# Performance work log

Hardware: AMD Instinct MI355X
Metric: run time of the kernel (lower is better)

Reference implementation:

```python
import jax, jax.numpy as jnp
import numpy as np

B, L, S, H, E = 4, 2048, 2048, 8, 64

def setup_inputs() -> dict:
    key = jax.random.key(0)
    kq, kk, kv, kt, kd = jax.random.split(key, 5)
    return {
        "queries": jax.random.normal(kq, (B, L, H, E), dtype=jnp.float32),
        "keys": jax.random.normal(kk, (B, S, H, E), dtype=jnp.float32),
        "values": jax.random.normal(kv, (B, S, H, E), dtype=jnp.float32),
        "attn_mask": jnp.zeros((1,), dtype=bool),
        "tau": jax.random.uniform(kt, (B, 1), dtype=jnp.float32),
        "delta": jax.random.normal(kd, (B, 1), dtype=jnp.float32),
    }

def reference(queries, keys, values, attn_mask, tau, delta):
    # queries: [B,L,H,E], keys: [B,S,H,E], values: [B,S,H,D]
    Bq, Lq, Hq, Eq = queries.shape
    scale = 1.0 / jnp.sqrt(jnp.float32(Eq))
    scores = jnp.einsum('blhe,bshe->bhls', queries, keys)  # [B,H,L,S]
    scores = scores * tau.reshape(Bq, 1, 1, 1)             # per-batch tau scale
    scores = scores + delta.reshape(Bq, 1, 1, 1)           # per-batch delta bias
    A = jax.nn.softmax(scale * scores, axis=-1)            # dropout is identity at eval
    V = jnp.einsum('bhls,bshd->blhd', A, values)           # [B,L,H,D]
    return V
```

## Files before the change

### kernel.cpp

```cpp
#include <hip/hip_runtime.h>
#include <hip/hip_bf16.h>
#include <stdint.h>

#define LL 2048
#define SS 2048
#define HH 8
#define EE 64
#define RSG 512

typedef float v4f __attribute__((ext_vector_type(4)));
typedef short s4v __attribute__((ext_vector_type(4)));
typedef short s8v __attribute__((ext_vector_type(8)));

__device__ __forceinline__ short f2bf(float f) {
    unsigned u = __float_as_uint(f);
    u = (u + 0x7fffu + ((u >> 16) & 1u)) >> 16;
    return (short)u;
}

__device__ __forceinline__ s4v pack4bf(float a, float b, float c, float d) {
    float2 ab = make_float2(a, b), cd = make_float2(c, d);
    __hip_bfloat162 r0 = __float22bfloat162_rn(ab);
    __hip_bfloat162 r1 = __float22bfloat162_rn(cd);
    s4v r;
    __builtin_memcpy(&r, &r0, 4);
    __builtin_memcpy(((char*)&r) + 4, &r1, 4);
    return r;
}

__global__ __launch_bounds__(256)
void dsattn_prep(const float* __restrict__ kk, const float* __restrict__ vv,
                 short* __restrict__ kbf, short* __restrict__ vimg)
{
    __shared__ float T[64][68];
    const int t = threadIdx.x;
    const int blk = blockIdx.x;
    if (blk < 1024) {
        const float* src = kk + (size_t)blk * 4096;
        short* dst = kbf + (size_t)blk * 4096;
        #pragma unroll
        for (int c = 0; c < 4; ++c) {
            v4f d = *(const v4f*)(src + (c * 256 + t) * 4);
            *(s4v*)(dst + (c * 256 + t) * 4) = pack4bf(d[0], d[1], d[2], d[3]);
        }
    } else {
        const int vb = blk - 1024;
        const int b = vb >> 8, h = (vb >> 5) & 7, ts = vb & 31;
        const float* vp = vv + ((size_t)b * SS + ts * 64) * RSG + h * EE;
        #pragma unroll
        for (int c = 0; c < 4; ++c) {
            int idx = c * 256 + t, s = idx >> 4, e0 = (idx & 15) << 2;
            *(v4f*)&T[s][e0] = *(const v4f*)(vp + (size_t)s * RSG + e0);
        }
        __syncthreads();
        short* dst = vimg + (size_t)vb * 4096;
        #pragma unroll
        for (int half = 0; half < 2; ++half) {
            int ci = half * 256 + t;
            int e = ci >> 3, sc = ci & 7;
            int c = sc ^ (e & 7);
            s8v ov;
            #pragma unroll
            for (int m = 0; m < 8; ++m) {
                int s = 16 * (m & 3) + 2 * c + (m >> 2);
                ov[m] = f2bf(T[s][e]);
            }
            *(s8v*)(dst + ci * 8) = ov;
        }
    }
}

__global__ __launch_bounds__(256, 2)
void dsattn_main(const float* __restrict__ q, const short* __restrict__ kbf,
                 const short* __restrict__ vimg, const float* __restrict__ tau,
                 const float* __restrict__ delta, float* __restrict__ out)
{
    __shared__ short KV[2][8192];
    __shared__ short Ps[128 * 64];

    const int t    = threadIdx.x;
    const int lane = t & 63;
    const int w    = t >> 6;
    const int l15  = lane & 15;
    const int l4   = lane >> 4;
    const int mt = blockIdx.x, h = blockIdx.y, b = blockIdx.z;

    const float LOG2E = 1.44269504088896f;
    const float sc2 = 0.125f * LOG2E * tau[b];
    const float dl2 = 0.125f * LOG2E * delta[b];

    s8v qf[2][2];
    {
        const float* qb = q + ((size_t)b * LL + (size_t)mt * 128 + w * 32) * RSG + h * EE;
        #pragma unroll
        for (int mb = 0; mb < 2; ++mb) {
            const float* qr = qb + (size_t)(mb * 16 + l15) * RSG + l4 * 8;
            v4f a0 = *(const v4f*)(qr);
            v4f a1 = *(const v4f*)(qr + 4);
            v4f a2 = *(const v4f*)(qr + 32);
            v4f a3 = *(const v4f*)(qr + 36);
            s4v p0 = pack4bf(a0[0], a0[1], a0[2], a0[3]);
            s4v p1 = pack4bf(a1[0], a1[1], a1[2], a1[3]);
            s4v p2 = pack4bf(a2[0], a2[1], a2[2], a2[3]);
            s4v p3 = pack4bf(a3[0], a3[1], a3[2], a3[3]);
            s8v f0, f1;
            #pragma unroll
            for (int j = 0; j < 4; ++j) { f0[j] = p0[j]; f0[4 + j] = p1[j]; f1[j] = p2[j]; f1[4 + j] = p3[j]; }
            qf[mb][0] = f0; qf[mb][1] = f1;
        }
    }

    const char* gsrc;
    int jstr, tstr;
    if (w < 2) {
        int i = w * 256 + lane;
        int row = i >> 3;
        int c = (i & 7) ^ (row & 7);
        gsrc = (const char*)(kbf + (size_t)b * (SS * RSG) + h * EE) + row * (RSG * 2) + c * 16;
        jstr = 8 * RSG * 2;
        tstr = 64 * RSG * 2;
    } else {
        int i2 = (w - 2) * 256 + lane;
        gsrc = (const char*)(vimg + (((size_t)b * HH + h) * 32) * 4096) + i2 * 16;
        jstr = 1024; tstr = 8192;
    }

    #define STAGE(p)                                                                    \
        {                                                                               \
            _Pragma("unroll")                                                           \
            for (int j = 0; j < 4; ++j) {                                               \
                __builtin_amdgcn_global_load_lds(                                       \
                    (const __attribute__((address_space(1))) unsigned*)(gsrc + j * jstr), \
                    (__attribute__((address_space(3))) unsigned*)&KV[p][w * 2048 + j * 512], \
                    16, 0, 0);                                                          \
            }                                                                           \
            gsrc += tstr;                                                               \
        }

    v4f oacc[2][4];
    float rs[2][4];
    #pragma unroll
    for (int mb = 0; mb < 2; ++mb)
        #pragma unroll
        for (int nb = 0; nb < 4; ++nb) {
            v4f z = {0.f, 0.f, 0.f, 0.f};
            oacc[mb][nb] = z;
            rs[mb][nb] = 0.f;
        }

    STAGE(0);

    for (int it = 0; it < 32; ++it) {
        const int p = it & 1;
        __syncthreads();
        if (it < 31) STAGE(p ^ 1);

        const short* Kp = &KV[p][0];
        const short* Vp = &KV[p][4096];

        v4f st[2][4];
        #pragma unroll
        for (int sb = 0; sb < 4; ++sb) {
            int sr = l15 + 16 * sb;
            int xo = sr & 7;
            s8v b0 = *(const s8v*)&Kp[sr * 64 + ((l4 ^ xo) << 3)];
            s8v b1 = *(const s8v*)&Kp[sr * 64 + (((l4 + 4) ^ xo) << 3)];
            #pragma unroll
            for (int mb = 0; mb < 2; ++mb) {
                v4f z = {0.f, 0.f, 0.f, 0.f};
                v4f a = __builtin_amdgcn_mfma_f32_16x16x32_bf16(qf[mb][0], b0, z, 0, 0, 0);
                st[mb][sb] = __builtin_amdgcn_mfma_f32_16x16x32_bf16(qf[mb][1], b1, a, 0, 0, 0);
            }
        }

        #pragma unroll
        for (int mb = 0; mb < 2; ++mb) {
            #pragma unroll
            for (int sb = 0; sb < 4; ++sb)
                #pragma unroll
                for (int r = 0; r < 4; ++r)
                    st[mb][sb][r] = __builtin_amdgcn_exp2f(st[mb][sb][r] * sc2 + dl2);
            #pragma unroll
            for (int r = 0; r < 4; ++r) {
                rs[mb][r] += (st[mb][0][r] + st[mb][1][r]) + (st[mb][2][r] + st[mb][3][r]);
                s4v pk = pack4bf(st[mb][0][r], st[mb][1][r], st[mb][2][r], st[mb][3][r]);
                int prow = w * 32 + mb * 16 + (l4 << 2) + r;
                int sc = (l15 >> 1) ^ (prow & 7);
                *(s4v*)&Ps[prow * 64 + (sc << 3) + ((l15 & 1) << 2)] = pk;
            }
        }

        s8v pf[2][2];
        #pragma unroll
        for (int mb = 0; mb < 2; ++mb) {
            int prow = w * 32 + mb * 16 + l15;
            int xo = prow & 7;
            pf[mb][0] = *(const s8v*)&Ps[prow * 64 + ((l4 ^ xo) << 3)];
            pf[mb][1] = *(const s8v*)&Ps[prow * 64 + (((l4 + 4) ^ xo) << 3)];
        }
        #pragma unroll
        for (int nb = 0; nb < 4; ++nb) {
            int e = l15 + 16 * nb;
            int xo = e & 7;
            s8v v0 = *(const s8v*)&Vp[e * 64 + ((l4 ^ xo) << 3)];
            s8v v1 = *(const s8v*)&Vp[e * 64 + (((l4 + 4) ^ xo) << 3)];
            #pragma unroll
            for (int mb = 0; mb < 2; ++mb) {
                oacc[mb][nb] = __builtin_amdgcn_mfma_f32_16x16x32_bf16(pf[mb][0], v0, oacc[mb][nb], 0, 0, 0);
                oacc[mb][nb] = __builtin_amdgcn_mfma_f32_16x16x32_bf16(pf[mb][1], v1, oacc[mb][nb], 0, 0, 0);
            }
        }
    }

    #pragma unroll
    for (int mb = 0; mb < 2; ++mb)
        #pragma unroll
        for (int r = 0; r < 4; ++r) {
            float v = rs[mb][r];
            v += __shfl_xor(v, 1);
            v += __shfl_xor(v, 2);
            v += __shfl_xor(v, 4);
            v += __shfl_xor(v, 8);
            rs[mb][r] = 1.0f / v;
        }
    float* ob = out + ((size_t)b * LL + (size_t)mt * 128 + w * 32) * RSG + h * EE;
    #pragma unroll
    for (int mb = 0; mb < 2; ++mb)
        #pragma unroll
        for (int r = 0; r < 4; ++r) {
            int row = mb * 16 + (l4 << 2) + r;
            float inv = rs[mb][r];
            #pragma unroll
            for (int nb = 0; nb < 4; ++nb)
                ob[(size_t)row * RSG + l15 + 16 * nb] = oacc[mb][nb][r] * inv;
        }
}

extern "C" void kernel_launch(void* const* d_in, const int* in_sizes, int n_in,
                              void* d_out, int out_size, void* d_ws, size_t ws_size,
                              hipStream_t stream) {
    const float* q     = (const float*)d_in[0];
    const float* k     = (const float*)d_in[1];
    const float* v     = (const float*)d_in[2];
    const float* tau   = (const float*)d_in[4];
    const float* delta = (const float*)d_in[5];
    float* out = (float*)d_out;

    short* kbf  = (short*)d_ws;
    short* vimg = kbf + (size_t)4 * SS * RSG;

    dsattn_prep<<<dim3(2048), dim3(256), 0, stream>>>(k, v, kbf, vimg);
    dsattn_main<<<dim3(LL / 128, HH, 4), dim3(256), 0, stream>>>(q, kbf, vimg, tau, delta, out);
}
```

Measured before the change: 150.0 us.

## Switch to transposed 32x32x16 MFMA keeping P in registers, fold scale into Q

Replaces the 16x16x32 MFMA tiling with 32x32x16 MFMAs that compute S^T = K·Q^T, so each lane holds a full query column and the exp'd scores can be repacked directly as the B operand of the PV MFMA. This removes the shared-memory round trip for P and its barrier-free LDS traffic, and reduces the row-sum reduction to one cross-half shuffle. The softmax scale and tau are folded into Q before bf16 conversion, and delta is dropped because a constant per-batch bias cancels in softmax. The V prep layout is reordered to match the new operand layout, and pre-scaling Q before rounding to bf16 slightly changes rounding.

```diff
diff --git a/kernel.cpp b/kernel.cpp
--- a/kernel.cpp
+++ b/kernel.cpp
@@ -8,9 +8,10 @@
 #define EE 64
 #define RSG 512
 
-typedef float v4f __attribute__((ext_vector_type(4)));
-typedef short s4v __attribute__((ext_vector_type(4)));
-typedef short s8v __attribute__((ext_vector_type(8)));
+typedef float v4f  __attribute__((ext_vector_type(4)));
+typedef float v16f __attribute__((ext_vector_type(16)));
+typedef short s4v  __attribute__((ext_vector_type(4)));
+typedef short s8v  __attribute__((ext_vector_type(8)));
 
 __device__ __forceinline__ short f2bf(float f) {
     unsigned u = __float_as_uint(f);
@@ -57,13 +58,14 @@
         #pragma unroll
         for (int half = 0; half < 2; ++half) {
             int ci = half * 256 + t;
-            int e = ci >> 3, sc = ci & 7;
-            int c = sc ^ (e & 7);
+            int e = ci >> 3, pos = ci & 7;
+            int c = pos ^ (e & 7);
+            int sbase = 16 * (c >> 1) + 4 * (c & 1);
             s8v ov;
             #pragma unroll
-            for (int m = 0; m < 8; ++m) {
-                int s = 16 * (m & 3) + 2 * c + (m >> 2);
-                ov[m] = f2bf(T[s][e]);
+            for (int j = 0; j < 8; ++j) {
+                int s = sbase + 8 * (j >> 2) + (j & 3);
+                ov[j] = f2bf(T[s][e]);
             }
             *(s8v*)(dst + ci * 8) = ov;
         }
@@ -73,40 +75,33 @@
 __global__ __launch_bounds__(256, 2)
 void dsattn_main(const float* __restrict__ q, const short* __restrict__ kbf,
                  const short* __restrict__ vimg, const float* __restrict__ tau,
-                 const float* __restrict__ delta, float* __restrict__ out)
+                 float* __restrict__ out)
 {
     __shared__ short KV[2][8192];
-    __shared__ short Ps[128 * 64];
 
     const int t    = threadIdx.x;
     const int lane = t & 63;
     const int w    = t >> 6;
-    const int l15  = lane & 15;
-    const int l4   = lane >> 4;
+    const int l31  = lane & 31;
+    const int hi   = lane >> 5;
     const int mt = blockIdx.x, h = blockIdx.y, b = blockIdx.z;
 
-    const float LOG2E = 1.44269504088896f;
-    const float sc2 = 0.125f * LOG2E * tau[b];
-    const float dl2 = 0.125f * LOG2E * delta[b];
-
-    s8v qf[2][2];
+    const float scf = 0.125f * 1.44269504088896f * tau[b];
+
+    s8v qf[4];
     {
-        const float* qb = q + ((size_t)b * LL + (size_t)mt * 128 + w * 32) * RSG + h * EE;
-        #pragma unroll
-        for (int mb = 0; mb < 2; ++mb) {
-            const float* qr = qb + (size_t)(mb * 16 + l15) * RSG + l4 * 8;
-            v4f a0 = *(const v4f*)(qr);
-            v4f a1 = *(const v4f*)(qr + 4);
-            v4f a2 = *(const v4f*)(qr + 32);
-            v4f a3 = *(const v4f*)(qr + 36);
-            s4v p0 = pack4bf(a0[0], a0[1], a0[2], a0[3]);
-            s4v p1 = pack4bf(a1[0], a1[1], a1[2], a1[3]);
-            s4v p2 = pack4bf(a2[0], a2[1], a2[2], a2[3]);
-            s4v p3 = pack4bf(a3[0], a3[1], a3[2], a3[3]);
-            s8v f0, f1;
-            #pragma unroll
-            for (int j = 0; j < 4; ++j) { f0[j] = p0[j]; f0[4 + j] = p1[j]; f1[j] = p2[j]; f1[4 + j] = p3[j]; }
-            qf[mb][0] = f0; qf[mb][1] = f1;
+        const float* qb = q + ((size_t)b * LL + (size_t)mt * 128 + w * 32 + l31) * RSG
+                            + h * EE + 8 * hi;
+        #pragma unroll
+        for (int ks = 0; ks < 4; ++ks) {
+            v4f a0 = *(const v4f*)(qb + 16 * ks);
+            v4f a1 = *(const v4f*)(qb + 16 * ks + 4);
+            s4v p0 = pack4bf(a0[0] * scf, a0[1] * scf, a0[2] * scf, a0[3] * scf);
+            s4v p1 = pack4bf(a1[0] * scf, a1[1] * scf, a1[2] * scf, a1[3] * scf);
+            s8v f;
+            #pragma unroll
+            for (int j = 0; j < 4; ++j) { f[j] = p0[j]; f[4 + j] = p1[j]; }
+            qf[ks] = f;
         }
     }
 
@@ -125,28 +120,30 @@
         jstr = 1024; tstr = 8192;
     }
 
-    #define STAGE(p)                                                                    \
-        {                                                                               \
-            _Pragma("unroll")                                                           \
-            for (int j = 0; j < 4; ++j) {                                               \
-                __builtin_amdgcn_global_load_lds(                                       \
+    #define STAGE(p)                                                                      \
+        {                                                                                 \
+            _Pragma("unroll")                                                             \
+            for (int j = 0; j < 4; ++j) {                                                 \
+                __builtin_amdgcn_global_load_lds(                                         \
                     (const __attribute__((address_space(1))) unsigned*)(gsrc + j * jstr), \
                     (__attribute__((address_space(3))) unsigned*)&KV[p][w * 2048 + j * 512], \
-                    16, 0, 0);                                                          \
-            }                                                                           \
-            gsrc += tstr;                                                               \
-        }
-
-    v4f oacc[2][4];
-    float rs[2][4];
+                    16, 0, 0);                                                            \
+            }                                                                             \
+            gsrc += tstr;                                                                 \
+        }
+
+    v16f oacc[2];
     #pragma unroll
     for (int mb = 0; mb < 2; ++mb)
         #pragma unroll
-        for (int nb = 0; nb < 4; ++nb) {
-            v4f z = {0.f, 0.f, 0.f, 0.f};
-            oacc[mb][nb] = z;
-            rs[mb][nb] = 0.f;
-        }
+        for (int r = 0; r < 16; ++r) oacc[mb][r] = 0.0f;
+    float rsum = 0.0f;
+
+    const int xo = l31 & 7;
+    const int rbase = l31 * 64;
+    int kpos[4];
+    #pragma unroll
+    for (int ks = 0; ks < 4; ++ks) kpos[ks] = (((hi + 2 * ks) & 7) ^ xo) * 8;
 
     STAGE(0);
 
@@ -158,81 +155,66 @@
         const short* Kp = &KV[p][0];
         const short* Vp = &KV[p][4096];
 
-        v4f st[2][4];
-        #pragma unroll
-        for (int sb = 0; sb < 4; ++sb) {
-            int sr = l15 + 16 * sb;
-            int xo = sr & 7;
-            s8v b0 = *(const s8v*)&Kp[sr * 64 + ((l4 ^ xo) << 3)];
-            s8v b1 = *(const s8v*)&Kp[sr * 64 + (((l4 + 4) ^ xo) << 3)];
-            #pragma unroll
-            for (int mb = 0; mb < 2; ++mb) {
-                v4f z = {0.f, 0.f, 0.f, 0.f};
-                v4f a = __builtin_amdgcn_mfma_f32_16x16x32_bf16(qf[mb][0], b0, z, 0, 0, 0);
-                st[mb][sb] = __builtin_amdgcn_mfma_f32_16x16x32_bf16(qf[mb][1], b1, a, 0, 0, 0);
+        v16f st[2];
+        #pragma unroll
+        for (int mb = 0; mb < 2; ++mb) {
+            v16f z;
+            #pragma unroll
+            for (int r = 0; r < 16; ++r) z[r] = 0.0f;
+            #pragma unroll
+            for (int ks = 0; ks < 4; ++ks) {
+                s8v kf = *(const s8v*)&Kp[mb * 2048 + rbase + kpos[ks]];
+                z = __builtin_amdgcn_mfma_f32_32x32x16_bf16(kf, qf[ks], z, 0, 0, 0);
             }
+            st[mb] = z;
+        }
+
+        #pragma unroll
+        for (int mb = 0; mb < 2; ++mb)
+            #pragma unroll
+            for (int r = 0; r < 16; ++r)
+                st[mb][r] = __builtin_amdgcn_exp2f(st[mb][r]);
+        float s0 = 0.f, s1 = 0.f;
+        #pragma unroll
+        for (int r = 0; r < 16; ++r) { s0 += st[0][r]; s1 += st[1][r]; }
+        rsum += s0 + s1;
+
+        s8v pf[4];
+        #pragma unroll
+        for (int tt = 0; tt < 4; ++tt) {
+            int o = 8 * (tt & 1);
+            const v16f& sv = st[tt >> 1];
+            s4v lo = pack4bf(sv[o + 0], sv[o + 1], sv[o + 2], sv[o + 3]);
+            s4v hs = pack4bf(sv[o + 4], sv[o + 5], sv[o + 6], sv[o + 7]);
+            s8v f;
+            #pragma unroll
+            for (int j = 0; j < 4; ++j) { f[j] = lo[j]; f[4 + j] = hs[j]; }
+            pf[tt] = f;
         }
 
         #pragma unroll
         for (int mb = 0; mb < 2; ++mb) {
-            #pragma unroll
-            for (int sb = 0; sb < 4; ++sb)
-                #pragma unroll
-                for (int r = 0; r < 4; ++r)
-                    st[mb][sb][r] = __builtin_amdgcn_exp2f(st[mb][sb][r] * sc2 + dl2);
-            #pragma unroll
-            for (int r = 0; r < 4; ++r) {
-                rs[mb][r] += (st[mb][0][r] + st[mb][1][r]) + (st[mb][2][r] + st[mb][3][r]);
-                s4v pk = pack4bf(st[mb][0][r], st[mb][1][r], st[mb][2][r], st[mb][3][r]);
-                int prow = w * 32 + mb * 16 + (l4 << 2) + r;
-                int sc = (l15 >> 1) ^ (prow & 7);
-                *(s4v*)&Ps[prow * 64 + (sc << 3) + ((l15 & 1) << 2)] = pk;
+            v16f acc = oacc[mb];
+            #pragma unroll
+            for (int ks = 0; ks < 4; ++ks) {
+                s8v vf = *(const s8v*)&Vp[mb * 2048 + rbase + kpos[ks]];
+                acc = __builtin_amdgcn_mfma_f32_32x32x16_bf16(vf, pf[ks], acc, 0, 0, 0);
             }
-        }
-
-        s8v pf[2][2];
-        #pragma unroll
-        for (int mb = 0; mb < 2; ++mb) {
-            int prow = w * 32 + mb * 16 + l15;
-            int xo = prow & 7;
-            pf[mb][0] = *(const s8v*)&Ps[prow * 64 + ((l4 ^ xo) << 3)];
-            pf[mb][1] = *(const s8v*)&Ps[prow * 64 + (((l4 + 4) ^ xo) << 3)];
-        }
-        #pragma unroll
-        for (int nb = 0; nb < 4; ++nb) {
-            int e = l15 + 16 * nb;
-            int xo = e & 7;
-            s8v v0 = *(const s8v*)&Vp[e * 64 + ((l4 ^ xo) << 3)];
-            s8v v1 = *(const s8v*)&Vp[e * 64 + (((l4 + 4) ^ xo) << 3)];
-            #pragma unroll
-            for (int mb = 0; mb < 2; ++mb) {
-                oacc[mb][nb] = __builtin_amdgcn_mfma_f32_16x16x32_bf16(pf[mb][0], v0, oacc[mb][nb], 0, 0, 0);
-                oacc[mb][nb] = __builtin_amdgcn_mfma_f32_16x16x32_bf16(pf[mb][1], v1, oacc[mb][nb], 0, 0, 0);
-            }
-        }
-    }
-
+            oacc[mb] = acc;
+        }
+    }
+
+    rsum += __shfl_xor(rsum, 32);
+    const float inv = 1.0f / rsum;
+    float* ob = out + ((size_t)b * LL + (size_t)mt * 128 + w * 32 + l31) * RSG + h * EE;
     #pragma unroll
     for (int mb = 0; mb < 2; ++mb)
         #pragma unroll
-        for (int r = 0; r < 4; ++r) {
-            float v = rs[mb][r];
-            v += __shfl_xor(v, 1);
-            v += __shfl_xor(v, 2);
-            v += __shfl_xor(v, 4);
-            v += __shfl_xor(v, 8);
-            rs[mb][r] = 1.0f / v;
-        }
-    float* ob = out + ((size_t)b * LL + (size_t)mt * 128 + w * 32) * RSG + h * EE;
-    #pragma unroll
-    for (int mb = 0; mb < 2; ++mb)
-        #pragma unroll
-        for (int r = 0; r < 4; ++r) {
-            int row = mb * 16 + (l4 << 2) + r;
-            float inv = rs[mb][r];
-            #pragma unroll
-            for (int nb = 0; nb < 4; ++nb)
-                ob[(size_t)row * RSG + l15 + 16 * nb] = oacc[mb][nb][r] * inv;
+        for (int rq = 0; rq < 4; ++rq) {
+            int e0 = 32 * mb + 8 * rq + 4 * hi;
+            v4f o4 = { oacc[mb][4 * rq + 0] * inv, oacc[mb][4 * rq + 1] * inv,
+                       oacc[mb][4 * rq + 2] * inv, oacc[mb][4 * rq + 3] * inv };
+            *(v4f*)(ob + e0) = o4;
         }
 }
 
@@ -243,12 +225,11 @@
     const float* k     = (const float*)d_in[1];
     const float* v     = (const float*)d_in[2];
     const float* tau   = (const float*)d_in[4];
-    const float* delta = (const float*)d_in[5];
     float* out = (float*)d_out;
 
     short* kbf  = (short*)d_ws;
     short* vimg = kbf + (size_t)4 * SS * RSG;
 
     dsattn_prep<<<dim3(2048), dim3(256), 0, stream>>>(k, v, kbf, vimg);
-    dsattn_main<<<dim3(LL / 128, HH, 4), dim3(256), 0, stream>>>(q, kbf, vimg, tau, delta, out);
-}
+    dsattn_main<<<dim3(LL / 128, HH, 4), dim3(256), 0, stream>>>(q, kbf, vimg, tau, out);
+}
```

Measured after the change: 135.9 us. 1.1x faster.
